# Kernel tuning notes

Hardware: AMD Instinct MI355X
Metric: run time of the kernel (lower is better)

## Reference

```python
import jax, jax.numpy as jnp
import numpy as np

B, S, H, DH, DM = 1024, 32, 32, 32, 1024  # seq==heads==head_dim==32 forced by module's reshapes


def setup_inputs() -> dict:
    key = jax.random.key(0)
    k1, k2 = jax.random.split(key)
    x = jax.random.normal(k1, (B, S, DM), dtype=jnp.float32)
    mask = jnp.ones((1, 1, S, DH), dtype=bool)
    W_qkv = jax.random.normal(k2, (DM, 3 * H * DH), dtype=jnp.float32) / np.sqrt(DM).astype(np.float32)
    return {"x": x, "mask": mask, "W_qkv": W_qkv}


def _rope(t, sin, cos):
    # t: [B, S, H, DH]; sin/cos: [S] broadcast over the HEADS axis (axis 2), as in the original
    t1, t2 = jnp.split(t, 2, axis=-1)
    rot = jnp.concatenate([-t2, t1], axis=-1)
    return t * cos.reshape(1, 1, -1, 1) + rot * sin.reshape(1, 1, -1, 1)


def reference(x, mask, W_qkv):
    b, seq_len, _ = x.shape
    qkv = x @ W_qkv  # [B, S, 3*H*DH]
    q, k, v = jnp.split(qkv, 3, axis=-1)
    q = q.reshape(b, -1, H, DH)
    k = k.reshape(b, -1, H, DH)
    v = v.reshape(b, -1, H, DH)
    pos = jnp.arange(seq_len, dtype=x.dtype)
    sin, cos = jnp.sin(pos), jnp.cos(pos)
    q = _rope(q, sin, cos)
    k = _rope(k, sin, cos)
    # matmul over heads axis (faithful to original): [B,S,H,DH] @ [B,S,DH,H] -> [B,S,H,H]
    attn = jnp.matmul(q, k.transpose(0, 1, 3, 2)) / jnp.sqrt(jnp.asarray(DH, x.dtype))
    attn = attn.reshape(b, H, seq_len, DH)  # valid only because H == 32
    attn = jnp.where(jnp.broadcast_to(mask, attn.shape), attn, -jnp.inf)
    attn = jax.nn.softmax(attn, axis=-1)
    out = jnp.matmul(attn, v)  # [B,H,S,DH] @ [B,S,H,DH]; batched since S==H==32
    return out.reshape(-1, seq_len, H * DH)
```

## Files before the change

kernel.cpp:

```cpp
#include <hip/hip_runtime.h>

typedef __bf16 bf16_t;
typedef __bf16 bf16x4 __attribute__((ext_vector_type(4)));
typedef __bf16 bf16x8 __attribute__((ext_vector_type(8)));
typedef float f32x4 __attribute__((ext_vector_type(4)));
typedef float f32x16 __attribute__((ext_vector_type(16)));
typedef unsigned int uint4v __attribute__((ext_vector_type(4)));

#define M_TOT 32768
#define N_TOT 3072
#define K_TOT 1024

#define WT_BYTES (3072u * 1024u * 2u)
#define XB_BYTES ((size_t)M_TOT * 1024 * 2)

#define SLOT 32768

__device__ __forceinline__ void gload_lds16(const void* g, void* l) {
  __builtin_amdgcn_global_load_lds(
      (const __attribute__((address_space(1))) unsigned int*)g,
      (__attribute__((address_space(3))) unsigned int*)l, 16, 0, 0);
}

__device__ __forceinline__ unsigned pk2(float a, float b) {
  unsigned short lo = __builtin_bit_cast(unsigned short, (bf16_t)a);
  unsigned short hi = __builtin_bit_cast(unsigned short, (bf16_t)b);
  return ((unsigned)hi << 16) | (unsigned)lo;
}

__global__ __launch_bounds__(256) void k_prep(const float* __restrict__ x,
                                              const float* __restrict__ W,
                                              bf16_t* __restrict__ xb,
                                              bf16_t* __restrict__ wt) {
  const int bid = blockIdx.x;
  const int t = threadIdx.x;
  if (bid < 768) {
    __shared__ float tile[64][65];
    const int c0 = (bid % 48) * 64, k0 = (bid / 48) * 64;
    for (int rep = 0; rep < 16; ++rep) {
      int lin = rep * 256 + t;
      int kl = lin >> 6, cl = lin & 63;
      tile[kl][cl] = W[(size_t)(k0 + kl) * 3072 + (c0 + cl)];
    }
    __syncthreads();
    const float scale = 0.17677669529663687f;
    for (int rep = 0; rep < 16; ++rep) {
      int lin = rep * 256 + t;
      int cl = lin >> 6, kl = lin & 63;
      int c = c0 + cl;
      float val;
      if (c < 2048) {
        int cc = c & 1023;
        int h = cc >> 5, d = cc & 31;
        float cv = cosf((float)h), sv = sinf((float)h);
        int clp = cl + ((d < 16) ? 16 : -16);
        float other = tile[kl][clp];
        val = tile[kl][cl] * cv + ((d < 16) ? -other : other) * sv;
        if (c < 1024) val *= scale;
      } else {
        val = tile[kl][cl];
      }
      wt[(size_t)c * 1024 + (k0 + kl)] = (bf16_t)val;
    }
  } else {
    const size_t nf4 = (size_t)M_TOT * K_TOT / 4;
    const float4* src = (const float4*)x;
    for (size_t i = (size_t)(bid - 768) * 256 + t; i < nf4; i += (size_t)16384 * 256) {
      float4 a = src[i];
      bf16x4 o;
      o[0] = (bf16_t)a.x; o[1] = (bf16_t)a.y; o[2] = (bf16_t)a.z; o[3] = (bf16_t)a.w;
      *(bf16x4*)(&xb[i * 4]) = o;
    }
  }
}

template <int STG>
__device__ __forceinline__ void kt(const char* sR, const char* sN, char* sW,
                                   const char* pS, int dstOff,
                                   int aoff, int boff,
                                   f32x4 (&acc)[8][4],
                                   bf16x8 (&aQ1)[4], bf16x8 (&bC)[4],
                                   bf16x8 (&bN)[4]) {
  bf16x8 aQ2[4];
  if constexpr (STG == 1) {
    gload_lds16(pS, sW + dstOff);
    gload_lds16(pS + 32768, sW + dstOff + 1024);
  }
#pragma unroll
  for (int i = 0; i < 4; ++i)
    aQ2[i] = *(const bf16x8*)(sR + aoff + (4 + i) * 2048);
  asm volatile("s_waitcnt lgkmcnt(4)" ::: "memory");
  __builtin_amdgcn_sched_barrier(0);
  __builtin_amdgcn_s_setprio(1);
#pragma unroll
  for (int m = 0; m < 4; ++m)
#pragma unroll
    for (int n = 0; n < 4; ++n)
      acc[m][n] = __builtin_amdgcn_mfma_f32_16x16x32_bf16(aQ1[m], bC[n], acc[m][n], 0, 0, 0);
  __builtin_amdgcn_s_setprio(0);
  if constexpr (STG == 1) {
    gload_lds16(pS + 65536, sW + dstOff + 2048);
    gload_lds16(pS + 98304, sW + dstOff + 3072);
    asm volatile("s_waitcnt vmcnt(4)" ::: "memory");
  } else if constexpr (STG == 2) {
    asm volatile("s_waitcnt vmcnt(0)" ::: "memory");
  }
  asm volatile("s_waitcnt lgkmcnt(0)" ::: "memory");
  __builtin_amdgcn_sched_barrier(0);
  if constexpr (STG <= 2) {
    __builtin_amdgcn_s_barrier();
#pragma unroll
    for (int i = 0; i < 4; ++i) aQ1[i] = *(const bf16x8*)(sN + aoff + i * 2048);
#pragma unroll
    for (int i = 0; i < 4; ++i) bN[i] = *(const bf16x8*)(sN + boff + i * 4096);
    __builtin_amdgcn_sched_barrier(0);
  }
  __builtin_amdgcn_s_setprio(1);
#pragma unroll
  for (int m = 0; m < 4; ++m)
#pragma unroll
    for (int n = 0; n < 4; ++n)
      acc[m + 4][n] = __builtin_amdgcn_mfma_f32_16x16x32_bf16(aQ2[m], bC[n], acc[m + 4][n], 0, 0, 0);
  __builtin_amdgcn_s_setprio(0);
}

__global__ __launch_bounds__(512, 1) void k_gemm(const bf16_t* __restrict__ xb,
                                                 const bf16_t* __restrict__ wt,
                                                 bf16_t* __restrict__ qk,
                                                 bf16_t* __restrict__ vb) {
  __shared__ __attribute__((aligned(16))) char lds[3 * SLOT];
  const int tid = threadIdx.x;
  const int w = tid >> 6, lane = tid & 63;
  const int wr = w >> 2, wc = w & 3;

  const int bid = blockIdx.x;
  const int swz = (bid & 7) * 192 + (bid >> 3);
  const int tm = swz / 12, tn = swz % 12;
  const int row0 = tm * 256, col0 = tn * 256;

  const int isB = w >> 2;
  const int rL = (w & 3) * 64 + (lane >> 2);
  const int g = (lane & 3) ^ ((lane >> 3) & 3);
  const char* src = isB
      ? (const char*)wt + (size_t)(col0 + rL) * 2048 + g * 16
      : (const char*)xb + (size_t)(row0 + rL) * 2048 + g * 16;
  const int dstOff = (w & 3) * 4096 + isB * 16384;

  const int rsel = lane & 15, kslot = lane >> 4;
  const int kx = ((kslot ^ ((rsel >> 1) & 3)) << 4);
  const int aoff = (wr * 16 + rsel) * 64 + kx;
  const int boff = 16384 + (wc * 16 + rsel) * 64 + kx;

  f32x4 acc[8][4];
#pragma unroll
  for (int m = 0; m < 8; ++m)
#pragma unroll
    for (int n = 0; n < 4; ++n)
#pragma unroll
      for (int i = 0; i < 4; ++i) acc[m][n][i] = 0.f;

  bf16x8 aQ1[4], bX[4], bY[4];

  char* const S0 = lds;
  char* const S1 = lds + SLOT;
  char* const S2 = lds + 2 * SLOT;

  {
#pragma unroll
    for (int c = 0; c < 4; ++c) gload_lds16(src + c * 32768, S0 + dstOff + c * 1024);
#pragma unroll
    for (int c = 0; c < 4; ++c) gload_lds16(src + 64 + c * 32768, S1 + dstOff + c * 1024);
    asm volatile("s_waitcnt vmcnt(4)" ::: "memory");
    __builtin_amdgcn_s_barrier();
    __builtin_amdgcn_sched_barrier(0);
#pragma unroll
    for (int i = 0; i < 4; ++i) aQ1[i] = *(const bf16x8*)(S0 + aoff + i * 2048);
#pragma unroll
    for (int i = 0; i < 4; ++i) bX[i] = *(const bf16x8*)(S0 + boff + i * 4096);
  }

  const char* pS = src + 128;
  for (int i = 0; i < 5; ++i) {
    kt<1>(S0, S1, S2, pS,       dstOff, aoff, boff, acc, aQ1, bX, bY);
    kt<1>(S1, S2, S0, pS + 64,  dstOff, aoff, boff, acc, aQ1, bY, bX);
    kt<1>(S2, S0, S1, pS + 128, dstOff, aoff, boff, acc, aQ1, bX, bY);
    kt<1>(S0, S1, S2, pS + 192, dstOff, aoff, boff, acc, aQ1, bY, bX);
    kt<1>(S1, S2, S0, pS + 256, dstOff, aoff, boff, acc, aQ1, bX, bY);
    kt<1>(S2, S0, S1, pS + 320, dstOff, aoff, boff, acc, aQ1, bY, bX);
    pS += 384;
  }
  kt<2>(S0, S1, S2, pS, dstOff, aoff, boff, acc, aQ1, bX, bY);
  kt<3>(S1, S1, S2, pS, dstOff, aoff, boff, acc, aQ1, bY, bX);

  const bool isv = (col0 >= 2048);
  const int rgrp = kslot * 4;
#pragma unroll
  for (int m = 0; m < 8; ++m)
#pragma unroll
    for (int n = 0; n < 4; ++n)
#pragma unroll
      for (int reg = 0; reg < 4; ++reg) {
        const int R = row0 + wr * 16 + m * 32 + rgrp + reg;
        const int C = col0 + wc * 16 + n * 64 + rsel;
        const bf16_t val = (bf16_t)acc[m][n][reg];
        if (!isv) qk[(size_t)R * 2048 + C] = val;
        else      vb[(size_t)R * 1024 + (C - 2048)] = val;
      }
}

__global__ __launch_bounds__(256) void k_attn(const bf16_t* __restrict__ qk,
                                              const bf16_t* __restrict__ vb,
                                              float* __restrict__ out) {
  __shared__ __attribute__((aligned(16))) bf16_t vl[4][1024];
  const int t = threadIdx.x;
  const int w = t >> 6, lane = t & 63;
  const int r = blockIdx.x * 4 + w;
  const int jm = lane & 31, hi = lane >> 5;

  const char* vsrc = (const char*)vb + (size_t)r * 2048;
  gload_lds16(vsrc + lane * 16, (char*)vl[w]);
  gload_lds16(vsrc + 1024 + lane * 16, (char*)vl[w] + 1024);

  const char* rowbase = (const char*)qk + (size_t)r * 4096;
  const bf16x8 ak0 = *(const bf16x8*)(rowbase + 2048 + jm * 64 + hi * 16);
  const bf16x8 ak1 = *(const bf16x8*)(rowbase + 2048 + jm * 64 + 32 + hi * 16);
  const bf16x8 bq0 = *(const bf16x8*)(rowbase + jm * 64 + hi * 16);
  const bf16x8 bq1 = *(const bf16x8*)(rowbase + jm * 64 + 32 + hi * 16);

  f32x16 s;
  for (int i = 0; i < 16; ++i) s[i] = 0.f;
  s = __builtin_amdgcn_mfma_f32_32x32x16_bf16(ak0, bq0, s, 0, 0, 0);
  s = __builtin_amdgcn_mfma_f32_32x32x16_bf16(ak1, bq1, s, 0, 0, 0);

  float mx = s[0];
#pragma unroll
  for (int i = 1; i < 16; ++i) mx = fmaxf(mx, s[i]);
  mx = fmaxf(mx, __shfl_xor(mx, 32));
  float p[16];
  float sum = 0.f;
#pragma unroll
  for (int i = 0; i < 16; ++i) { p[i] = __expf(s[i] - mx); sum += p[i]; }
  sum += __shfl_xor(sum, 32);
  const float inv = 1.f / sum;
#pragma unroll
  for (int i = 0; i < 16; ++i) p[i] *= inv;

  const unsigned t01 = pk2(p[0], p[1]),  t23 = pk2(p[2], p[3]);
  const unsigned t45 = pk2(p[4], p[5]),  t67 = pk2(p[6], p[7]);
  const unsigned t89 = pk2(p[8], p[9]),  tab = pk2(p[10], p[11]);
  const unsigned tcd = pk2(p[12], p[13]), tef = pk2(p[14], p[15]);
  const unsigned x01 = (unsigned)__shfl_xor((int)t01, 32), x23 = (unsigned)__shfl_xor((int)t23, 32);
  const unsigned x45 = (unsigned)__shfl_xor((int)t45, 32), x67 = (unsigned)__shfl_xor((int)t67, 32);
  const unsigned x89 = (unsigned)__shfl_xor((int)t89, 32), xab = (unsigned)__shfl_xor((int)tab, 32);
  const unsigned xcd = (unsigned)__shfl_xor((int)tcd, 32), xef = (unsigned)__shfl_xor((int)tef, 32);
  uint4v u0, u1;
  u0[0] = hi ? x45 : t01; u0[1] = hi ? x67 : t23; u0[2] = hi ? t45 : x01; u0[3] = hi ? t67 : x23;
  u1[0] = hi ? xcd : t89; u1[1] = hi ? xef : tab; u1[2] = hi ? tcd : x89; u1[3] = hi ? tef : xab;
  const bf16x8 pa0 = __builtin_bit_cast(bf16x8, u0);
  const bf16x8 pa1 = __builtin_bit_cast(bf16x8, u1);

  asm volatile("s_waitcnt vmcnt(0)" ::: "memory");
  union { bf16x8 v; bf16_t e[8]; } v0, v1;
#pragma unroll
  for (int e = 0; e < 8; ++e) v0.e[e] = vl[w][(8 * hi + e) * 32 + jm];
#pragma unroll
  for (int e = 0; e < 8; ++e) v1.e[e] = vl[w][(16 + 8 * hi + e) * 32 + jm];

  f32x16 o;
  for (int i = 0; i < 16; ++i) o[i] = 0.f;
  o = __builtin_amdgcn_mfma_f32_32x32x16_bf16(pa0, v0.v, o, 0, 0, 0);
  o = __builtin_amdgcn_mfma_f32_32x32x16_bf16(pa1, v1.v, o, 0, 0, 0);

  float* orow = out + (size_t)r * 1024;
#pragma unroll
  for (int reg = 0; reg < 16; ++reg) {
    const int jrow = (reg & 3) + 8 * (reg >> 2) + 4 * hi;
    orow[jrow * 32 + jm] = o[reg];
  }
}

extern "C" void kernel_launch(void* const* d_in, const int* in_sizes, int n_in,
                              void* d_out, int out_size, void* d_ws, size_t ws_size,
                              hipStream_t stream) {
  const float* x = (const float*)d_in[0];
  const float* W = (const float*)d_in[2];

  char* ws = (char*)d_ws;
  bf16_t* wt = (bf16_t*)ws;
  bf16_t* xb = (bf16_t*)(ws + WT_BYTES);
  bf16_t* vb = (bf16_t*)(ws + WT_BYTES + XB_BYTES);

  k_prep<<<17152, 256, 0, stream>>>(x, W, xb, wt);
  k_gemm<<<1536, 512, 0, stream>>>(xb, wt, (bf16_t*)d_out, vb);
  k_attn<<<8192, 256, 0, stream>>>((const bf16_t*)d_out, vb, (float*)d_out);
}
```

Before: 290.2 us.

## Shrink GEMM tile to 256x128 with smaller LDS slots for higher occupancy

The QKV GEMM tile drops from 256x256 to 256x128, so each wave holds half as many accumulators and the grid doubles to 3072 blocks. LDS slots shrink to 24 KB and each wave now issues three direct-to-LDS loads per stage instead of four. The launch bound changes to allow several blocks per CU. The aim is to raise occupancy so latency is hidden across workgroups. The cost is lower arithmetic intensity per tile and more global traffic for re-reading the A operand.

```diff
diff --git a/kernel.cpp b/kernel.cpp
--- a/kernel.cpp
+++ b/kernel.cpp
@@ -14,7 +14,7 @@
 #define WT_BYTES (3072u * 1024u * 2u)
 #define XB_BYTES ((size_t)M_TOT * 1024 * 2)
 
-#define SLOT 32768
+#define SLOT 24576
 
 __device__ __forceinline__ void gload_lds16(const void* g, void* l) {
   __builtin_amdgcn_global_load_lds(
@@ -76,90 +76,92 @@
 
 template <int STG>
 __device__ __forceinline__ void kt(const char* sR, const char* sN, char* sW,
-                                   const char* pS, int dstOff,
+                                   const char* s0, const char* s1, const char* s2,
+                                   int d0, int d1, int d2,
                                    int aoff, int boff,
-                                   f32x4 (&acc)[8][4],
-                                   bf16x8 (&aQ1)[4], bf16x8 (&bC)[4],
-                                   bf16x8 (&bN)[4]) {
-  bf16x8 aQ2[4];
+                                   f32x4 (&acc)[4][4],
+                                   bf16x8 (&aQ1)[2], bf16x8 (&bC)[4]) {
+  bf16x8 aQ2[2];
   if constexpr (STG == 1) {
-    gload_lds16(pS, sW + dstOff);
-    gload_lds16(pS + 32768, sW + dstOff + 1024);
-  }
-#pragma unroll
-  for (int i = 0; i < 4; ++i)
-    aQ2[i] = *(const bf16x8*)(sR + aoff + (4 + i) * 2048);
-  asm volatile("s_waitcnt lgkmcnt(4)" ::: "memory");
+    gload_lds16(s0, sW + d0);
+    gload_lds16(s1, sW + d1);
+    gload_lds16(s2, sW + d2);
+  }
+  aQ2[0] = *(const bf16x8*)(sR + aoff + 8192);
+  aQ2[1] = *(const bf16x8*)(sR + aoff + 12288);
+  asm volatile("s_waitcnt lgkmcnt(2)" ::: "memory");
   __builtin_amdgcn_sched_barrier(0);
   __builtin_amdgcn_s_setprio(1);
 #pragma unroll
-  for (int m = 0; m < 4; ++m)
+  for (int m = 0; m < 2; ++m)
 #pragma unroll
     for (int n = 0; n < 4; ++n)
       acc[m][n] = __builtin_amdgcn_mfma_f32_16x16x32_bf16(aQ1[m], bC[n], acc[m][n], 0, 0, 0);
   __builtin_amdgcn_s_setprio(0);
-  if constexpr (STG == 1) {
-    gload_lds16(pS + 65536, sW + dstOff + 2048);
-    gload_lds16(pS + 98304, sW + dstOff + 3072);
-    asm volatile("s_waitcnt vmcnt(4)" ::: "memory");
-  } else if constexpr (STG == 2) {
-    asm volatile("s_waitcnt vmcnt(0)" ::: "memory");
-  }
+  if constexpr (STG == 1) asm volatile("s_waitcnt vmcnt(3)" ::: "memory");
+  else if constexpr (STG == 2) asm volatile("s_waitcnt vmcnt(0)" ::: "memory");
   asm volatile("s_waitcnt lgkmcnt(0)" ::: "memory");
   __builtin_amdgcn_sched_barrier(0);
   if constexpr (STG <= 2) {
     __builtin_amdgcn_s_barrier();
-#pragma unroll
-    for (int i = 0; i < 4; ++i) aQ1[i] = *(const bf16x8*)(sN + aoff + i * 2048);
-#pragma unroll
-    for (int i = 0; i < 4; ++i) bN[i] = *(const bf16x8*)(sN + boff + i * 4096);
+    aQ1[0] = *(const bf16x8*)(sN + aoff);
+    aQ1[1] = *(const bf16x8*)(sN + aoff + 4096);
     __builtin_amdgcn_sched_barrier(0);
   }
   __builtin_amdgcn_s_setprio(1);
 #pragma unroll
-  for (int m = 0; m < 4; ++m)
-#pragma unroll
-    for (int n = 0; n < 4; ++n)
-      acc[m + 4][n] = __builtin_amdgcn_mfma_f32_16x16x32_bf16(aQ2[m], bC[n], acc[m + 4][n], 0, 0, 0);
+  for (int m = 0; m < 2; ++m)
+#pragma unroll
+    for (int n = 0; n < 4; ++n)
+      acc[m + 2][n] = __builtin_amdgcn_mfma_f32_16x16x32_bf16(aQ2[m], bC[n], acc[m + 2][n], 0, 0, 0);
   __builtin_amdgcn_s_setprio(0);
-}
-
-__global__ __launch_bounds__(512, 1) void k_gemm(const bf16_t* __restrict__ xb,
+  if constexpr (STG <= 2) {
+#pragma unroll
+    for (int n = 0; n < 4; ++n)
+      bC[n] = *(const bf16x8*)(sN + boff + n * 2048);
+  }
+}
+
+__global__ __launch_bounds__(512, 4) void k_gemm(const bf16_t* __restrict__ xb,
                                                  const bf16_t* __restrict__ wt,
                                                  bf16_t* __restrict__ qk,
                                                  bf16_t* __restrict__ vb) {
   __shared__ __attribute__((aligned(16))) char lds[3 * SLOT];
   const int tid = threadIdx.x;
   const int w = tid >> 6, lane = tid & 63;
-  const int wr = w >> 2, wc = w & 3;
+  const int wr = w >> 1, wc = w & 1;
 
   const int bid = blockIdx.x;
-  const int swz = (bid & 7) * 192 + (bid >> 3);
-  const int tm = swz / 12, tn = swz % 12;
-  const int row0 = tm * 256, col0 = tn * 256;
-
-  const int isB = w >> 2;
-  const int rL = (w & 3) * 64 + (lane >> 2);
+  const int swz = (bid & 7) * 384 + (bid >> 3);
+  const int tm = swz / 24, tn = swz % 24;
+  const int row0 = tm * 256, col0 = tn * 128;
+
   const int g = (lane & 3) ^ ((lane >> 3) & 3);
-  const char* src = isB
-      ? (const char*)wt + (size_t)(col0 + rL) * 2048 + g * 16
-      : (const char*)xb + (size_t)(row0 + rL) * 2048 + g * 16;
-  const int dstOff = (w & 3) * 4096 + isB * 16384;
+  const char* srcs[3];
+  int dsts[3];
+#pragma unroll
+  for (int j = 0; j < 3; ++j) {
+    const int c = 3 * w + j;
+    const bool isB = c >= 16;
+    const int r = (isB ? col0 + (c - 16) * 16 : row0 + c * 16) + (lane >> 2);
+    srcs[j] = (isB ? (const char*)wt : (const char*)xb) + (size_t)r * 2048 + g * 16;
+    dsts[j] = c * 1024;
+  }
 
   const int rsel = lane & 15, kslot = lane >> 4;
   const int kx = ((kslot ^ ((rsel >> 1) & 3)) << 4);
   const int aoff = (wr * 16 + rsel) * 64 + kx;
   const int boff = 16384 + (wc * 16 + rsel) * 64 + kx;
 
-  f32x4 acc[8][4];
-#pragma unroll
-  for (int m = 0; m < 8; ++m)
+  f32x4 acc[4][4];
+#pragma unroll
+  for (int m = 0; m < 4; ++m)
 #pragma unroll
     for (int n = 0; n < 4; ++n)
 #pragma unroll
       for (int i = 0; i < 4; ++i) acc[m][n][i] = 0.f;
 
-  bf16x8 aQ1[4], bX[4], bY[4];
+  bf16x8 aQ1[2], bC[4];
 
   char* const S0 = lds;
   char* const S1 = lds + SLOT;
@@ -167,41 +169,41 @@
 
   {
 #pragma unroll
-    for (int c = 0; c < 4; ++c) gload_lds16(src + c * 32768, S0 + dstOff + c * 1024);
-#pragma unroll
-    for (int c = 0; c < 4; ++c) gload_lds16(src + 64 + c * 32768, S1 + dstOff + c * 1024);
-    asm volatile("s_waitcnt vmcnt(4)" ::: "memory");
+    for (int j = 0; j < 3; ++j) gload_lds16(srcs[j], S0 + dsts[j]);
+#pragma unroll
+    for (int j = 0; j < 3; ++j) gload_lds16(srcs[j] + 64, S1 + dsts[j]);
+    asm volatile("s_waitcnt vmcnt(3)" ::: "memory");
     __builtin_amdgcn_s_barrier();
     __builtin_amdgcn_sched_barrier(0);
-#pragma unroll
-    for (int i = 0; i < 4; ++i) aQ1[i] = *(const bf16x8*)(S0 + aoff + i * 2048);
-#pragma unroll
-    for (int i = 0; i < 4; ++i) bX[i] = *(const bf16x8*)(S0 + boff + i * 4096);
-  }
-
-  const char* pS = src + 128;
-  for (int i = 0; i < 5; ++i) {
-    kt<1>(S0, S1, S2, pS,       dstOff, aoff, boff, acc, aQ1, bX, bY);
-    kt<1>(S1, S2, S0, pS + 64,  dstOff, aoff, boff, acc, aQ1, bY, bX);
-    kt<1>(S2, S0, S1, pS + 128, dstOff, aoff, boff, acc, aQ1, bX, bY);
-    kt<1>(S0, S1, S2, pS + 192, dstOff, aoff, boff, acc, aQ1, bY, bX);
-    kt<1>(S1, S2, S0, pS + 256, dstOff, aoff, boff, acc, aQ1, bX, bY);
-    kt<1>(S2, S0, S1, pS + 320, dstOff, aoff, boff, acc, aQ1, bY, bX);
-    pS += 384;
-  }
-  kt<2>(S0, S1, S2, pS, dstOff, aoff, boff, acc, aQ1, bX, bY);
-  kt<3>(S1, S1, S2, pS, dstOff, aoff, boff, acc, aQ1, bY, bX);
+    aQ1[0] = *(const bf16x8*)(S0 + aoff);
+    aQ1[1] = *(const bf16x8*)(S0 + aoff + 4096);
+#pragma unroll
+    for (int n = 0; n < 4; ++n) bC[n] = *(const bf16x8*)(S0 + boff + n * 2048);
+  }
+
+  const char* p0 = srcs[0] + 128;
+  const char* p1 = srcs[1] + 128;
+  const char* p2 = srcs[2] + 128;
+  const int d0 = dsts[0], d1 = dsts[1], d2 = dsts[2];
+  for (int i = 0; i < 10; ++i) {
+    kt<1>(S0, S1, S2, p0,       p1,       p2,       d0, d1, d2, aoff, boff, acc, aQ1, bC);
+    kt<1>(S1, S2, S0, p0 + 64,  p1 + 64,  p2 + 64,  d0, d1, d2, aoff, boff, acc, aQ1, bC);
+    kt<1>(S2, S0, S1, p0 + 128, p1 + 128, p2 + 128, d0, d1, d2, aoff, boff, acc, aQ1, bC);
+    p0 += 192; p1 += 192; p2 += 192;
+  }
+  kt<2>(S0, S1, S2, p0, p1, p2, d0, d1, d2, aoff, boff, acc, aQ1, bC);
+  kt<3>(S1, S2, S0, p0, p1, p2, d0, d1, d2, aoff, boff, acc, aQ1, bC);
 
   const bool isv = (col0 >= 2048);
   const int rgrp = kslot * 4;
 #pragma unroll
-  for (int m = 0; m < 8; ++m)
+  for (int m = 0; m < 4; ++m)
 #pragma unroll
     for (int n = 0; n < 4; ++n)
 #pragma unroll
       for (int reg = 0; reg < 4; ++reg) {
-        const int R = row0 + wr * 16 + m * 32 + rgrp + reg;
-        const int C = col0 + wc * 16 + n * 64 + rsel;
+        const int R = row0 + wr * 16 + m * 64 + rgrp + reg;
+        const int C = col0 + wc * 16 + n * 32 + rsel;
         const bf16_t val = (bf16_t)acc[m][n][reg];
         if (!isv) qk[(size_t)R * 2048 + C] = val;
         else      vb[(size_t)R * 1024 + (C - 2048)] = val;
@@ -291,6 +293,6 @@
   bf16_t* vb = (bf16_t*)(ws + WT_BYTES + XB_BYTES);
 
   k_prep<<<17152, 256, 0, stream>>>(x, W, xb, wt);
-  k_gemm<<<1536, 512, 0, stream>>>(xb, wt, (bf16_t*)d_out, vb);
+  k_gemm<<<3072, 512, 0, stream>>>(xb, wt, (bf16_t*)d_out, vb);
   k_attn<<<8192, 256, 0, stream>>>((const bf16_t*)d_out, vb, (float*)d_out);
 }
```

After: 317.2 us. 1.09x slower.

## Switch QKV GEMM to 32x32x16 MFMA tiles with new register fragment layout

Applied to the files above, without the earlier changes.

Replaces the 16x16x32 bf16 MFMA inner product with 32x32x16 MFMA instructions, changing each wave's sub-tile mapping, LDS fragment offsets (with XOR swizzle for the two k-halves), accumulator layout and the epilogue store indexing. It also reorders the B-fragment reload to after the second MFMA batch and simplifies the unrolled K loop to a 3-stage rotation. The larger MFMA shape cuts LDS reads per FLOP and instruction count, at the cost of a different bank-access pattern and output store layout that must match exactly.

```diff
diff --git a/kernel.cpp b/kernel.cpp
--- a/kernel.cpp
+++ b/kernel.cpp
@@ -78,25 +78,27 @@
 __device__ __forceinline__ void kt(const char* sR, const char* sN, char* sW,
                                    const char* pS, int dstOff,
                                    int aoff, int boff,
-                                   f32x4 (&acc)[8][4],
-                                   bf16x8 (&aQ1)[4], bf16x8 (&bC)[4],
-                                   bf16x8 (&bN)[4]) {
-  bf16x8 aQ2[4];
+                                   f32x16 (&acc)[4][2],
+                                   bf16x8 (&aC)[2][2], bf16x8 (&bC)[2][2]) {
+  bf16x8 aH[2][2];
   if constexpr (STG == 1) {
     gload_lds16(pS, sW + dstOff);
     gload_lds16(pS + 32768, sW + dstOff + 1024);
   }
-#pragma unroll
-  for (int i = 0; i < 4; ++i)
-    aQ2[i] = *(const bf16x8*)(sR + aoff + (4 + i) * 2048);
+  aH[0][0] = *(const bf16x8*)(sR + (aoff + 8192));
+  aH[0][1] = *(const bf16x8*)(sR + ((aoff + 8192) ^ 32));
+  aH[1][0] = *(const bf16x8*)(sR + (aoff + 12288));
+  aH[1][1] = *(const bf16x8*)(sR + ((aoff + 12288) ^ 32));
   asm volatile("s_waitcnt lgkmcnt(4)" ::: "memory");
   __builtin_amdgcn_sched_barrier(0);
   __builtin_amdgcn_s_setprio(1);
 #pragma unroll
-  for (int m = 0; m < 4; ++m)
-#pragma unroll
-    for (int n = 0; n < 4; ++n)
-      acc[m][n] = __builtin_amdgcn_mfma_f32_16x16x32_bf16(aQ1[m], bC[n], acc[m][n], 0, 0, 0);
+  for (int mt = 0; mt < 2; ++mt)
+#pragma unroll
+    for (int nt = 0; nt < 2; ++nt) {
+      acc[mt][nt] = __builtin_amdgcn_mfma_f32_32x32x16_bf16(aC[mt][0], bC[nt][0], acc[mt][nt], 0, 0, 0);
+      acc[mt][nt] = __builtin_amdgcn_mfma_f32_32x32x16_bf16(aC[mt][1], bC[nt][1], acc[mt][nt], 0, 0, 0);
+    }
   __builtin_amdgcn_s_setprio(0);
   if constexpr (STG == 1) {
     gload_lds16(pS + 65536, sW + dstOff + 2048);
@@ -109,19 +111,27 @@
   __builtin_amdgcn_sched_barrier(0);
   if constexpr (STG <= 2) {
     __builtin_amdgcn_s_barrier();
-#pragma unroll
-    for (int i = 0; i < 4; ++i) aQ1[i] = *(const bf16x8*)(sN + aoff + i * 2048);
-#pragma unroll
-    for (int i = 0; i < 4; ++i) bN[i] = *(const bf16x8*)(sN + boff + i * 4096);
+    aC[0][0] = *(const bf16x8*)(sN + aoff);
+    aC[0][1] = *(const bf16x8*)(sN + (aoff ^ 32));
+    aC[1][0] = *(const bf16x8*)(sN + (aoff + 4096));
+    aC[1][1] = *(const bf16x8*)(sN + ((aoff + 4096) ^ 32));
     __builtin_amdgcn_sched_barrier(0);
   }
   __builtin_amdgcn_s_setprio(1);
 #pragma unroll
-  for (int m = 0; m < 4; ++m)
-#pragma unroll
-    for (int n = 0; n < 4; ++n)
-      acc[m + 4][n] = __builtin_amdgcn_mfma_f32_16x16x32_bf16(aQ2[m], bC[n], acc[m + 4][n], 0, 0, 0);
+  for (int mt = 0; mt < 2; ++mt)
+#pragma unroll
+    for (int nt = 0; nt < 2; ++nt) {
+      acc[mt + 2][nt] = __builtin_amdgcn_mfma_f32_32x32x16_bf16(aH[mt][0], bC[nt][0], acc[mt + 2][nt], 0, 0, 0);
+      acc[mt + 2][nt] = __builtin_amdgcn_mfma_f32_32x32x16_bf16(aH[mt][1], bC[nt][1], acc[mt + 2][nt], 0, 0, 0);
+    }
   __builtin_amdgcn_s_setprio(0);
+  if constexpr (STG <= 2) {
+    bC[0][0] = *(const bf16x8*)(sN + boff);
+    bC[0][1] = *(const bf16x8*)(sN + (boff ^ 32));
+    bC[1][0] = *(const bf16x8*)(sN + (boff + 8192));
+    bC[1][1] = *(const bf16x8*)(sN + ((boff + 8192) ^ 32));
+  }
 }
 
 __global__ __launch_bounds__(512, 1) void k_gemm(const bf16_t* __restrict__ xb,
@@ -146,20 +156,20 @@
       : (const char*)xb + (size_t)(row0 + rL) * 2048 + g * 16;
   const int dstOff = (w & 3) * 4096 + isB * 16384;
 
-  const int rsel = lane & 15, kslot = lane >> 4;
-  const int kx = ((kslot ^ ((rsel >> 1) & 3)) << 4);
-  const int aoff = (wr * 16 + rsel) * 64 + kx;
-  const int boff = 16384 + (wc * 16 + rsel) * 64 + kx;
-
-  f32x4 acc[8][4];
-#pragma unroll
-  for (int m = 0; m < 8; ++m)
-#pragma unroll
-    for (int n = 0; n < 4; ++n)
-#pragma unroll
-      for (int i = 0; i < 4; ++i) acc[m][n][i] = 0.f;
-
-  bf16x8 aQ1[4], bX[4], bY[4];
+  const int r32 = lane & 31, khalf = lane >> 5;
+  const int kx0 = ((khalf ^ ((r32 >> 1) & 3)) << 4);
+  const int aoff = (wr * 32 + r32) * 64 + kx0;
+  const int boff = 16384 + (wc * 32 + r32) * 64 + kx0;
+
+  f32x16 acc[4][2];
+#pragma unroll
+  for (int mt = 0; mt < 4; ++mt)
+#pragma unroll
+    for (int nt = 0; nt < 2; ++nt)
+#pragma unroll
+      for (int i = 0; i < 16; ++i) acc[mt][nt][i] = 0.f;
+
+  bf16x8 aC[2][2], bC[2][2];
 
   char* const S0 = lds;
   char* const S1 = lds + SLOT;
@@ -173,36 +183,37 @@
     asm volatile("s_waitcnt vmcnt(4)" ::: "memory");
     __builtin_amdgcn_s_barrier();
     __builtin_amdgcn_sched_barrier(0);
-#pragma unroll
-    for (int i = 0; i < 4; ++i) aQ1[i] = *(const bf16x8*)(S0 + aoff + i * 2048);
-#pragma unroll
-    for (int i = 0; i < 4; ++i) bX[i] = *(const bf16x8*)(S0 + boff + i * 4096);
+    aC[0][0] = *(const bf16x8*)(S0 + aoff);
+    aC[0][1] = *(const bf16x8*)(S0 + (aoff ^ 32));
+    aC[1][0] = *(const bf16x8*)(S0 + (aoff + 4096));
+    aC[1][1] = *(const bf16x8*)(S0 + ((aoff + 4096) ^ 32));
+    bC[0][0] = *(const bf16x8*)(S0 + boff);
+    bC[0][1] = *(const bf16x8*)(S0 + (boff ^ 32));
+    bC[1][0] = *(const bf16x8*)(S0 + (boff + 8192));
+    bC[1][1] = *(const bf16x8*)(S0 + ((boff + 8192) ^ 32));
   }
 
   const char* pS = src + 128;
-  for (int i = 0; i < 5; ++i) {
-    kt<1>(S0, S1, S2, pS,       dstOff, aoff, boff, acc, aQ1, bX, bY);
-    kt<1>(S1, S2, S0, pS + 64,  dstOff, aoff, boff, acc, aQ1, bY, bX);
-    kt<1>(S2, S0, S1, pS + 128, dstOff, aoff, boff, acc, aQ1, bX, bY);
-    kt<1>(S0, S1, S2, pS + 192, dstOff, aoff, boff, acc, aQ1, bY, bX);
-    kt<1>(S1, S2, S0, pS + 256, dstOff, aoff, boff, acc, aQ1, bX, bY);
-    kt<1>(S2, S0, S1, pS + 320, dstOff, aoff, boff, acc, aQ1, bY, bX);
-    pS += 384;
-  }
-  kt<2>(S0, S1, S2, pS, dstOff, aoff, boff, acc, aQ1, bX, bY);
-  kt<3>(S1, S1, S2, pS, dstOff, aoff, boff, acc, aQ1, bY, bX);
+  for (int i = 0; i < 10; ++i) {
+    kt<1>(S0, S1, S2, pS,       dstOff, aoff, boff, acc, aC, bC);
+    kt<1>(S1, S2, S0, pS + 64,  dstOff, aoff, boff, acc, aC, bC);
+    kt<1>(S2, S0, S1, pS + 128, dstOff, aoff, boff, acc, aC, bC);
+    pS += 192;
+  }
+  kt<2>(S0, S1, S2, pS, dstOff, aoff, boff, acc, aC, bC);
+  kt<3>(S1, S1, S2, pS, dstOff, aoff, boff, acc, aC, bC);
 
   const bool isv = (col0 >= 2048);
-  const int rgrp = kslot * 4;
-#pragma unroll
-  for (int m = 0; m < 8; ++m)
-#pragma unroll
-    for (int n = 0; n < 4; ++n)
-#pragma unroll
-      for (int reg = 0; reg < 4; ++reg) {
-        const int R = row0 + wr * 16 + m * 32 + rgrp + reg;
-        const int C = col0 + wc * 16 + n * 64 + rsel;
-        const bf16_t val = (bf16_t)acc[m][n][reg];
+#pragma unroll
+  for (int mt = 0; mt < 4; ++mt)
+#pragma unroll
+    for (int nt = 0; nt < 2; ++nt)
+#pragma unroll
+      for (int reg = 0; reg < 16; ++reg) {
+        const int rowin = (reg & 3) + 8 * (reg >> 2) + 4 * khalf;
+        const int R = row0 + wr * 32 + mt * 64 + rowin;
+        const int C = col0 + wc * 32 + nt * 128 + r32;
+        const bf16_t val = (bf16_t)acc[mt][nt][reg];
         if (!isv) qk[(size_t)R * 2048 + C] = val;
         else      vb[(size_t)R * 1024 + (C - 2048)] = val;
       }
```

Result: slower. 306.4 us (+5.6%).
